# Kernel optimization log

Measured on AMD Instinct MI355X. Metric: run time of the kernel, lower is better.

Reference implementation:

```python
import jax, jax.numpy as jnp
import numpy as np

N, C, K, H = 100000, 128, 16, 4
D = C // H
EPS = 1e-5


def _gelu(x):
    return jax.nn.gelu(x, approximate=False)


def _ln(x, g, b):
    mu = jnp.mean(x, axis=-1, keepdims=True)
    var = jnp.var(x, axis=-1, keepdims=True)
    return (x - mu) * jax.lax.rsqrt(var + EPS) * g + b


def setup_inputs() -> dict:
    key = jax.random.key(0)
    ks = jax.random.split(key, 24)
    s = 0.02
    inp = {
        "feat": jax.random.normal(ks[0], (N, C), jnp.float32),
        "coords": jax.random.normal(ks[1], (N, 3), jnp.float32),
        "knn_idx": jax.random.randint(ks[2], (N, K), 0, N, jnp.int32),
        "Wq": jax.random.normal(ks[3], (C, C), jnp.float32) * s,
        "bq": jnp.zeros((C,), jnp.float32),
        "Wk": jax.random.normal(ks[4], (C, C), jnp.float32) * s,
        "bk": jnp.zeros((C,), jnp.float32),
        "Wv": jax.random.normal(ks[5], (C, C), jnp.float32) * s,
        "bv": jnp.zeros((C,), jnp.float32),
        "Wp1": jax.random.normal(ks[6], (3, C), jnp.float32) * s,
        "bp1": jnp.zeros((C,), jnp.float32),
        "Wp2": jax.random.normal(ks[7], (C, C), jnp.float32) * s,
        "bp2": jnp.zeros((C,), jnp.float32),
        "Wo": jax.random.normal(ks[8], (C, C), jnp.float32) * s,
        "bo": jnp.zeros((C,), jnp.float32),
        "g1": jnp.ones((C,), jnp.float32),
        "b1": jnp.zeros((C,), jnp.float32),
        "Wf1": jax.random.normal(ks[9], (C, 2 * C), jnp.float32) * s,
        "bf1": jnp.zeros((2 * C,), jnp.float32),
        "Wf2": jax.random.normal(ks[10], (2 * C, C), jnp.float32) * s,
        "bf2": jnp.zeros((C,), jnp.float32),
        "g2": jnp.ones((C,), jnp.float32),
        "b2": jnp.zeros((C,), jnp.float32),
    }
    return inp


def reference(feat, coords, knn_idx, Wq, bq, Wk, bk, Wv, bv, Wp1, bp1, Wp2, bp2,
              Wo, bo, g1, b1, Wf1, bf1, Wf2, bf2, g2, b2):
    q = feat @ Wq + bq                      # (N, C)
    k_feat = feat @ Wk + bk
    v_feat = feat @ Wv + bv
    k_nbr = k_feat[knn_idx]                 # (N, K, C) irregular gather
    v_nbr = v_feat[knn_idx]
    rel_pos = coords[knn_idx] - coords[:, None, :]   # (N, K, 3)
    pe = _gelu(rel_pos @ Wp1 + bp1) @ Wp2 + bp2      # (N, K, C)
    k_nbr = (k_nbr + pe).reshape(N, K, H, D)
    v_nbr = (v_nbr + pe).reshape(N, K, H, D)
    qh = q.reshape(N, H, D)
    attn = jnp.einsum('nhd,nkhd->nhk', qh, k_nbr) / jnp.sqrt(jnp.float32(D))
    attn = jax.nn.softmax(attn, axis=-1)    # softmax over the K neighbors
    out = jnp.einsum('nhk,nkhd->nhd', attn, v_nbr).reshape(N, C)
    out = out @ Wo + bo
    x = _ln(feat + out, g1, b1)
    ffn = _gelu(x @ Wf1 + bf1) @ Wf2 + bf2
    return _ln(x + ffn, g2, b2)
```

## Files before the change

### kernel.cpp

```cpp
#include <hip/hip_runtime.h>
#include <math.h>

#define NPTS 100000
#define KNN  16
#define CH   50000
#define NCHUNK 2
#define ATT_BLOCKS 1280

typedef unsigned short bf16;
typedef __attribute__((ext_vector_type(8))) short bf16x8;
typedef __attribute__((ext_vector_type(4))) float f32x4;

__device__ __forceinline__ float bf2f(bf16 v) {
    union { unsigned int u; float f; } x; x.u = ((unsigned int)v) << 16; return x.f;
}
__device__ __forceinline__ bf16 f2bf(float f) {
    union { float f; unsigned int u; } x; x.f = f;
    unsigned int r = (x.u + 0x7FFFu + ((x.u >> 16) & 1u)) >> 16;
    return (bf16)r;
}
__device__ __forceinline__ unsigned int pack_bf16(float lo, float hi) {
    union { float f; unsigned int u; } a, b; a.f = lo; b.f = hi;
    return ((b.u + 0x8000u) & 0xffff0000u) | ((a.u + 0x8000u) >> 16);
}
__device__ __forceinline__ float f_lo(unsigned int u) {
    union { unsigned int x; float f; } c; c.x = u << 16; return c.f;
}
__device__ __forceinline__ float f_hi(unsigned int u) {
    union { unsigned int x; float f; } c; c.x = u & 0xffff0000u; return c.f;
}
__device__ __forceinline__ float ld1(const float* p) { return *p; }
__device__ __forceinline__ float ld1(const bf16* p) { return bf2f(*p); }

__device__ __forceinline__ float gelu_f(float x) {
    return 0.5f * x * (1.0f + erff(x * 0.70710678118654752f));
}
__device__ __forceinline__ float gelu_poly(float t) {
    float w = t * t;
    float poly = fmaf(w, fmaf(w, 0.025f, -0.16666667f), 1.0f);
    return t * fmaf(0.3989423f * t, poly, 0.5f);
}

__global__ void prep1_kernel(const float* __restrict__ Wp2, const float* __restrict__ Wo,
                             const float* __restrict__ bo, const float* __restrict__ bp2,
                             const float* __restrict__ bq, const float* __restrict__ bk,
                             const float* __restrict__ bv,
                             float* __restrict__ Wcat2, float* __restrict__ bo2,
                             float* __restrict__ bcat) {
    int b = blockIdx.x, t = threadIdx.x;
    if (b < 512) {
        int h = b >> 7, j = b & 127;
        float s = 0.f;
        for (int d = 0; d < 32; d++)
            s += Wp2[j * 128 + h * 32 + d] * Wo[(h * 32 + d) * 128 + t];
        Wcat2[b * 128 + t] = s;
    } else if (b == 512) {
        float s = bo[t];
        for (int c = 0; c < 128; c++) s += bp2[c] * Wo[c * 128 + t];
        bo2[t] = s;
    } else {
        bcat[t] = bq[t]; bcat[128 + t] = bk[t]; bcat[256 + t] = bv[t];
    }
}

__global__ void prep2_kernel(const float* __restrict__ Wq, const float* __restrict__ Wk,
                             const float* __restrict__ Wv, const float* __restrict__ Wp2,
                             const float* __restrict__ Wo, const float* __restrict__ Wcat2,
                             const float* __restrict__ Wf1, const float* __restrict__ Wf2,
                             bf16* __restrict__ BcatT, bf16* __restrict__ W2TT,
                             bf16* __restrict__ WcatT, bf16* __restrict__ Wf1T,
                             bf16* __restrict__ Wf2T) {
    int b = blockIdx.x, t = threadIdx.x;
    if (b < 384) {
        const float* W = (b < 128) ? Wq : (b < 256) ? Wk : Wv;
        BcatT[b * 128 + t] = f2bf(W[t * 128 + (b & 127)]);
    } else if (b < 512) {
        int idx = b - 384, h = idx >> 5, d = idx & 31;
        W2TT[h * 4096 + t * 32 + d] = f2bf(Wp2[t * 128 + h * 32 + d]);
    } else if (b < 640) {
        int j = b - 512;
        for (int i = 0; i < 5; i++) {
            int r = t + 128 * i;
            float v = (r < 128) ? Wo[r * 128 + j] : Wcat2[(r - 128) * 128 + j];
            WcatT[j * 640 + r] = f2bf(v);
        }
    } else if (b < 896) {
        int n = b - 640;
        Wf1T[n * 128 + t] = f2bf(Wf1[t * 256 + n]);
    } else {
        int n = b - 896;
        for (int i = 0; i < 2; i++) {
            int k = t + 128 * i;
            Wf2T[n * 256 + k] = f2bf(Wf2[k * 128 + n]);
        }
    }
}

__global__ __launch_bounds__(256) void qkv3_kernel(
    const float* __restrict__ A, const bf16* __restrict__ BT,
    const float* __restrict__ bias, bf16* __restrict__ C, int Nrows)
{
    __shared__ bf16 As[2][128 * 72];
    __shared__ bf16 Bs[2][128 * 72];

    const int tid = threadIdx.x;
    const int row0 = blockIdx.x * 128;
    const int wave = tid >> 6, wr = wave >> 1, wc = wave & 1;
    const int l = tid & 63, l15 = l & 15, g = l >> 4;
    const int sr = tid >> 1;
    const int sh = (tid & 1) * 32;

    {
        int row = row0 + sr;
#pragma unroll
        for (int h = 0; h < 2; h++) {
            uint4 t[4];
            if (row < Nrows) {
                const float* s = A + (size_t)row * 128 + h * 64 + sh;
#pragma unroll
                for (int j2 = 0; j2 < 4; j2++) {
                    float4 a = ((const float4*)s)[2 * j2];
                    float4 b = ((const float4*)s)[2 * j2 + 1];
                    union { uint4 u; ushort4 hh[2]; } c;
                    c.hh[0] = make_ushort4(f2bf(a.x), f2bf(a.y), f2bf(a.z), f2bf(a.w));
                    c.hh[1] = make_ushort4(f2bf(b.x), f2bf(b.y), f2bf(b.z), f2bf(b.w));
                    t[j2] = c.u;
                }
            } else {
#pragma unroll
                for (int j2 = 0; j2 < 4; j2++) t[j2] = make_uint4(0, 0, 0, 0);
            }
            bf16* dst = As[h] + sr * 72 + sh;
#pragma unroll
            for (int j2 = 0; j2 < 4; j2++) *(uint4*)(dst + 8 * j2) = t[j2];
        }
    }
    {
#pragma unroll
        for (int h = 0; h < 2; h++) {
            const bf16* s = BT + (size_t)sr * 128 + h * 64 + sh;
            bf16* dst = Bs[h] + sr * 72 + sh;
#pragma unroll
            for (int j2 = 0; j2 < 4; j2++)
                *(uint4*)(dst + 8 * j2) = ((const uint4*)s)[j2];
        }
    }
    __syncthreads();

    union FragU { uint2 q2[2]; bf16x8 v; };

    for (int z = 0; z < 3; z++) {
        f32x4 acc[4][4];
#pragma unroll
        for (int i = 0; i < 4; i++)
#pragma unroll
            for (int j = 0; j < 4; j++) acc[i][j] = (f32x4){0.f, 0.f, 0.f, 0.f};

#pragma unroll
        for (int h = 0; h < 2; h++) {
#pragma unroll
            for (int s2 = 0; s2 < 2; s2++) {
                bf16x8 af[4], bfr[4];
#pragma unroll
                for (int mt = 0; mt < 4; mt++) {
                    const bf16* p = As[h] + (wr * 64 + mt * 16 + l15) * 72 + s2 * 32 + 4 * g;
                    FragU u; u.q2[0] = *(const uint2*)p; u.q2[1] = *(const uint2*)(p + 16);
                    af[mt] = u.v;
                }
#pragma unroll
                for (int nt = 0; nt < 4; nt++) {
                    const bf16* p = Bs[h] + (wc * 64 + nt * 16 + l15) * 72 + s2 * 32 + 4 * g;
                    FragU u; u.q2[0] = *(const uint2*)p; u.q2[1] = *(const uint2*)(p + 16);
                    bfr[nt] = u.v;
                }
#pragma unroll
                for (int mt = 0; mt < 4; mt++)
#pragma unroll
                    for (int nt = 0; nt < 4; nt++)
                        acc[mt][nt] = __builtin_amdgcn_mfma_f32_16x16x32_bf16(
                            bfr[nt], af[mt], acc[mt][nt], 0, 0, 0);
            }
        }

        const int cg = 4 * g;
        bf16* Cz = C + (size_t)z * NPTS * 128;
        const float* bz = bias + z * 128;
#pragma unroll
        for (int nt = 0; nt < 4; nt++) {
            const int col = wc * 64 + nt * 16 + cg;
            float4 bv4 = *(const float4*)(bz + col);
#pragma unroll
            for (int mt = 0; mt < 4; mt++) {
                int row = row0 + wr * 64 + mt * 16 + l15;
                if (row < Nrows) {
                    float t0 = acc[mt][nt][0] + bv4.x;
                    float t1 = acc[mt][nt][1] + bv4.y;
                    float t2 = acc[mt][nt][2] + bv4.z;
                    float t3 = acc[mt][nt][3] + bv4.w;
                    uint2 u; u.x = pack_bf16(t0, t1); u.y = pack_bf16(t2, t3);
                    *(uint2*)(Cz + (size_t)row * 128 + col) = u;
                }
            }
        }
        __syncthreads();
        if (z < 2) {
#pragma unroll
            for (int h = 0; h < 2; h++) {
                const bf16* s = BT + (size_t)((z + 1) * 128 + sr) * 128 + h * 64 + sh;
                bf16* dst = Bs[h] + sr * 72 + sh;
#pragma unroll
                for (int j2 = 0; j2 < 4; j2++)
                    *(uint4*)(dst + 8 * j2) = ((const uint4*)s)[j2];
            }
            __syncthreads();
        }
    }
}

template<int EPI, bool SPLITA, typename TA, typename TC, typename TR>
__global__ __launch_bounds__(256) void mfma_gemm(
    const TA* __restrict__ A, const bf16* __restrict__ A2,
    const bf16* __restrict__ BT, const float* __restrict__ bias,
    const TR* __restrict__ resid, const float* __restrict__ gamma,
    const float* __restrict__ beta, TC* __restrict__ Cc,
    int Nrows, int Kdim, int lda, int ldc,
    int zA, int zBT, int zbias, int zC)
{
    __shared__ bf16 As[128 * 36];
    __shared__ bf16 Bs[128 * 36];

    const int tid = threadIdx.x;
    const int z = blockIdx.z;
    const TA* Ab = A + (size_t)z * zA;
    const bf16* BTb = BT + (size_t)z * zBT;
    const float* biasb = bias + (size_t)z * zbias;
    TC* Cb = Cc + (size_t)z * zC;

    const int row0 = blockIdx.x * 128;
    const int col0 = blockIdx.y * 128;
    const int wave = tid >> 6, wr = wave >> 1, wc = wave & 1;
    const int l = tid & 63, l15 = l & 15, g = l >> 4;
    const int ar = tid >> 1;
    const int ah = (tid & 1) * 16;

    f32x4 acc[4][4];
#pragma unroll
    for (int i = 0; i < 4; i++)
#pragma unroll
        for (int j = 0; j < 4; j++) acc[i][j] = (f32x4){0.f, 0.f, 0.f, 0.f};

    for (int k0 = 0; k0 < Kdim; k0 += 32) {
        {
            int row = row0 + ar;
            ushort4 tmp[4];
            if (row < Nrows) {
                const bf16* s = (const bf16*)Ab + (size_t)row * lda + k0 + ah;
#pragma unroll
                for (int j = 0; j < 4; j++) tmp[j] = ((const ushort4*)s)[j];
            } else {
#pragma unroll
                for (int j = 0; j < 4; j++) tmp[j] = make_ushort4(0, 0, 0, 0);
            }
#pragma unroll
            for (int j = 0; j < 4; j++)
                *(ushort4*)(As + ar * 36 + ah + 4 * j) = tmp[j];
        }
        {
            int n = col0 + ar;
            const bf16* s = BTb + (size_t)n * Kdim + k0 + ah;
#pragma unroll
            for (int j = 0; j < 4; j++)
                *(ushort4*)(Bs + ar * 36 + ah + 4 * j) = ((const ushort4*)s)[j];
        }
        __syncthreads();

        union FragU { uint2 q2[2]; bf16x8 v; };
        bf16x8 af[4], bfr[4];
#pragma unroll
        for (int mt = 0; mt < 4; mt++) {
            const bf16* p = As + (wr * 64 + mt * 16 + l15) * 36 + 4 * g;
            FragU u; u.q2[0] = *(const uint2*)p; u.q2[1] = *(const uint2*)(p + 16);
            af[mt] = u.v;
        }
#pragma unroll
        for (int nt = 0; nt < 4; nt++) {
            const bf16* p = Bs + (wc * 64 + nt * 16 + l15) * 36 + 4 * g;
            FragU u; u.q2[0] = *(const uint2*)p; u.q2[1] = *(const uint2*)(p + 16);
            bfr[nt] = u.v;
        }
#pragma unroll
        for (int mt = 0; mt < 4; mt++)
#pragma unroll
            for (int nt = 0; nt < 4; nt++)
                acc[mt][nt] = __builtin_amdgcn_mfma_f32_16x16x32_bf16(
                    bfr[nt], af[mt], acc[mt][nt], 0, 0, 0);
        __syncthreads();
    }

    const int cg = 4 * g;
#pragma unroll
    for (int nt = 0; nt < 4; nt++) {
        const int col = col0 + wc * 64 + nt * 16 + cg;
        float4 bv4 = make_float4(0.f, 0.f, 0.f, 0.f);
        if constexpr (EPI >= 1) bv4 = *(const float4*)(biasb + col);
#pragma unroll
        for (int mt = 0; mt < 4; mt++) {
            int row = row0 + wr * 64 + mt * 16 + l15;
            if (row < Nrows) {
                float t0 = acc[mt][nt][0], t1 = acc[mt][nt][1];
                float t2 = acc[mt][nt][2], t3 = acc[mt][nt][3];
                if constexpr (EPI >= 1) { t0 += bv4.x; t1 += bv4.y; t2 += bv4.z; t3 += bv4.w; }
                if constexpr (EPI == 2) { t0 = gelu_f(t0); t1 = gelu_f(t1); t2 = gelu_f(t2); t3 = gelu_f(t3); }
                if constexpr (sizeof(TC) == 2) {
                    uint2 u; u.x = pack_bf16(t0, t1); u.y = pack_bf16(t2, t3);
                    *(uint2*)((bf16*)Cb + (size_t)row * ldc + col) = u;
                } else {
                    *(float4*)((float*)Cb + (size_t)row * ldc + col) = make_float4(t0, t1, t2, t3);
                }
            }
        }
    }
}

template<int EPI, bool SPLITA, typename TA, typename TC, typename TR>
__global__ __launch_bounds__(256) void mfma_gemm64(
    const TA* __restrict__ A, const bf16* __restrict__ A2,
    const bf16* __restrict__ BT, const float* __restrict__ bias,
    const TR* __restrict__ resid, const float* __restrict__ gamma,
    const float* __restrict__ beta, TC* __restrict__ Cc,
    int Nrows, int Kdim, int lda, int ldc,
    int zA, int zBT, int zbias, int zC)
{
    __shared__ bf16 As[128 * 72];
    __shared__ bf16 Bs[128 * 72];
    __shared__ float reds[256], redq[256];
    __shared__ float mu[128], rstd[128];

    const int tid = threadIdx.x;
    const int z = blockIdx.z;
    const TA* Ab = A + (size_t)z * zA;
    const bf16* BTb = BT + (size_t)z * zBT;
    const float* biasb = bias + (size_t)z * zbias;
    TC* Cb = Cc + (size_t)z * zC;

    const int row0 = blockIdx.x * 128;
    const int col0 = blockIdx.y * 128;
    const int wave = tid >> 6, wr = wave >> 1, wc = wave & 1;
    const int l = tid & 63, l15 = l & 15, g = l >> 4;
    const int sr = tid >> 1;
    const int sh = (tid & 1) * 32;

    f32x4 acc[4][4];
#pragma unroll
    for (int i = 0; i < 4; i++)
#pragma unroll
        for (int j = 0; j < 4; j++) acc[i][j] = (f32x4){0.f, 0.f, 0.f, 0.f};

    for (int k0 = 0; k0 < Kdim; k0 += 64) {
        {
            int row = row0 + sr;
            uint4 t[4];
            if (row < Nrows) {
                if constexpr (SPLITA) {
                    const bf16* s = (k0 < 128)
                        ? ((const bf16*)Ab + (size_t)row * 128 + k0 + sh)
                        : (A2 + (size_t)row * 512 + (k0 - 128) + sh);
#pragma unroll
                    for (int j2 = 0; j2 < 4; j2++) t[j2] = ((const uint4*)s)[j2];
                } else if constexpr (sizeof(TA) == 4) {
                    const float* s = (const float*)Ab + (size_t)row * lda + k0 + sh;
#pragma unroll
                    for (int j2 = 0; j2 < 4; j2++) {
                        float4 a = ((const float4*)s)[2 * j2];
                        float4 b = ((const float4*)s)[2 * j2 + 1];
                        union { uint4 u; ushort4 h[2]; } c;
                        c.h[0] = make_ushort4(f2bf(a.x), f2bf(a.y), f2bf(a.z), f2bf(a.w));
                        c.h[1] = make_ushort4(f2bf(b.x), f2bf(b.y), f2bf(b.z), f2bf(b.w));
                        t[j2] = c.u;
                    }
                } else {
                    const bf16* s = (const bf16*)Ab + (size_t)row * lda + k0 + sh;
#pragma unroll
                    for (int j2 = 0; j2 < 4; j2++) t[j2] = ((const uint4*)s)[j2];
                }
            } else {
#pragma unroll
                for (int j2 = 0; j2 < 4; j2++) t[j2] = make_uint4(0, 0, 0, 0);
            }
            bf16* dst = As + sr * 72 + sh;
#pragma unroll
            for (int j2 = 0; j2 < 4; j2++) *(uint4*)(dst + 8 * j2) = t[j2];
        }
        {
            int nn = col0 + sr;
            const bf16* s = BTb + (size_t)nn * Kdim + k0 + sh;
            uint4 t[4];
#pragma unroll
            for (int j2 = 0; j2 < 4; j2++) t[j2] = ((const uint4*)s)[j2];
            bf16* dst = Bs + sr * 72 + sh;
#pragma unroll
            for (int j2 = 0; j2 < 4; j2++) *(uint4*)(dst + 8 * j2) = t[j2];
        }
        __syncthreads();

        union FragU { uint2 q2[2]; bf16x8 v; };
#pragma unroll
        for (int s = 0; s < 2; s++) {
            bf16x8 af[4], bfr[4];
#pragma unroll
            for (int mt = 0; mt < 4; mt++) {
                const bf16* p = As + (wr * 64 + mt * 16 + l15) * 72 + s * 32 + 4 * g;
                FragU u; u.q2[0] = *(const uint2*)p; u.q2[1] = *(const uint2*)(p + 16);
                af[mt] = u.v;
            }
#pragma unroll
            for (int nt = 0; nt < 4; nt++) {
                const bf16* p = Bs + (wc * 64 + nt * 16 + l15) * 72 + s * 32 + 4 * g;
                FragU u; u.q2[0] = *(const uint2*)p; u.q2[1] = *(const uint2*)(p + 16);
                bfr[nt] = u.v;
            }
#pragma unroll
            for (int mt = 0; mt < 4; mt++)
#pragma unroll
                for (int nt = 0; nt < 4; nt++)
                    acc[mt][nt] = __builtin_amdgcn_mfma_f32_16x16x32_bf16(
                        bfr[nt], af[mt], acc[mt][nt], 0, 0, 0);
        }
        __syncthreads();
    }

    const int cg = 4 * g;

    if constexpr (EPI != 3) {
#pragma unroll
        for (int nt = 0; nt < 4; nt++) {
            const int col = col0 + wc * 64 + nt * 16 + cg;
            float4 bv4 = make_float4(0.f, 0.f, 0.f, 0.f);
            if constexpr (EPI >= 1) bv4 = *(const float4*)(biasb + col);
#pragma unroll
            for (int mt = 0; mt < 4; mt++) {
                int row = row0 + wr * 64 + mt * 16 + l15;
                if (row < Nrows) {
                    float t0 = acc[mt][nt][0], t1 = acc[mt][nt][1];
                    float t2 = acc[mt][nt][2], t3 = acc[mt][nt][3];
                    if constexpr (EPI >= 1) { t0 += bv4.x; t1 += bv4.y; t2 += bv4.z; t3 += bv4.w; }
                    if constexpr (EPI == 2) { t0 = gelu_f(t0); t1 = gelu_f(t1); t2 = gelu_f(t2); t3 = gelu_f(t3); }
                    if constexpr (sizeof(TC) == 2) {
                        uint2 u; u.x = pack_bf16(t0, t1); u.y = pack_bf16(t2, t3);
                        *(uint2*)((bf16*)Cb + (size_t)row * ldc + col) = u;
                    } else {
                        *(float4*)((float*)Cb + (size_t)row * ldc + col) = make_float4(t0, t1, t2, t3);
                    }
                }
            }
        }
    } else {
        float4 bias4[4];
#pragma unroll
        for (int nt = 0; nt < 4; nt++)
            bias4[nt] = *(const float4*)(biasb + wc * 64 + nt * 16 + cg);
#pragma unroll
        for (int mt = 0; mt < 4; mt++) {
            int rl = wr * 64 + mt * 16 + l15;
            int row = row0 + rl;
            float s = 0.f, q = 0.f;
#pragma unroll
            for (int nt = 0; nt < 4; nt++) {
                const int col = wc * 64 + nt * 16 + cg;
                float rv0 = 0.f, rv1 = 0.f, rv2 = 0.f, rv3 = 0.f;
                if (row < Nrows) {
                    if constexpr (sizeof(TR) == 2) {
                        ushort4 rr = *(const ushort4*)((const bf16*)resid + (size_t)row * 128 + col);
                        rv0 = bf2f(rr.x); rv1 = bf2f(rr.y); rv2 = bf2f(rr.z); rv3 = bf2f(rr.w);
                    } else {
                        float4 rr = *(const float4*)((const float*)resid + (size_t)row * 128 + col);
                        rv0 = rr.x; rv1 = rr.y; rv2 = rr.z; rv3 = rr.w;
                    }
                }
                float t0 = acc[mt][nt][0] + bias4[nt].x + rv0;
                float t1 = acc[mt][nt][1] + bias4[nt].y + rv1;
                float t2 = acc[mt][nt][2] + bias4[nt].z + rv2;
                float t3 = acc[mt][nt][3] + bias4[nt].w + rv3;
                acc[mt][nt][0] = t0; acc[mt][nt][1] = t1;
                acc[mt][nt][2] = t2; acc[mt][nt][3] = t3;
                s += t0 + t1 + t2 + t3;
                q = fmaf(t0, t0, q); q = fmaf(t1, t1, q);
                q = fmaf(t2, t2, q); q = fmaf(t3, t3, q);
            }
            s += __shfl_xor(s, 16); s += __shfl_xor(s, 32);
            q += __shfl_xor(q, 16); q += __shfl_xor(q, 32);
            if ((l & 48) == 0) { reds[rl * 2 + wc] = s; redq[rl * 2 + wc] = q; }
        }
        __syncthreads();
        if (tid < 128) {
            float s = reds[tid * 2] + reds[tid * 2 + 1];
            float q = redq[tid * 2] + redq[tid * 2 + 1];
            float m = s * (1.f / 128.f);
            float v = q * (1.f / 128.f) - m * m;
            mu[tid] = m; rstd[tid] = rsqrtf(v + 1e-5f);
        }
        __syncthreads();
        float4 g4[4], b4[4];
#pragma unroll
        for (int nt = 0; nt < 4; nt++) {
            g4[nt] = *(const float4*)(gamma + wc * 64 + nt * 16 + cg);
            b4[nt] = *(const float4*)(beta + wc * 64 + nt * 16 + cg);
        }
#pragma unroll
        for (int mt = 0; mt < 4; mt++) {
            int rl = wr * 64 + mt * 16 + l15;
            int row = row0 + rl;
            if (row < Nrows) {
                float m = mu[rl], rd = rstd[rl];
#pragma unroll
                for (int nt = 0; nt < 4; nt++) {
                    const int col = wc * 64 + nt * 16 + cg;
                    float t0 = (acc[mt][nt][0] - m) * rd * g4[nt].x + b4[nt].x;
                    float t1 = (acc[mt][nt][1] - m) * rd * g4[nt].y + b4[nt].y;
                    float t2 = (acc[mt][nt][2] - m) * rd * g4[nt].z + b4[nt].z;
                    float t3 = (acc[mt][nt][3] - m) * rd * g4[nt].w + b4[nt].w;
                    if constexpr (sizeof(TC) == 2) {
                        uint2 u; u.x = pack_bf16(t0, t1); u.y = pack_bf16(t2, t3);
                        *(uint2*)((bf16*)Cb + (size_t)row * 128 + col) = u;
                    } else {
                        *(float4*)((float*)Cb + (size_t)row * 128 + col) = make_float4(t0, t1, t2, t3);
                    }
                }
            }
        }
    }
}

__global__ __launch_bounds__(256, 5) void attn_kernel(
    const bf16* __restrict__ qx, const bf16* __restrict__ kf,
    const bf16* __restrict__ vf, const bf16* __restrict__ qp,
    const float* __restrict__ coords, const int* __restrict__ knn,
    const float* __restrict__ Wp1, const float* __restrict__ bp1,
    bf16* __restrict__ attn_v, bf16* __restrict__ s_out, int nbase)
{
    __shared__ __align__(16) float W1s[524];
    __shared__ __align__(16) unsigned int hv_s[4][16 * 68];
    __shared__ __align__(16) float qp_s[4][4 * 144];
    __shared__ __align__(16) float a_s[4][64];
    __shared__ int idx_s[4][16];

    const int tid = threadIdx.x;
    if (tid < 128) {
        int c = tid;
        int s4 = 4 * c + 4 * (c >> 5);
        W1s[s4 + 0] = Wp1[c];
        W1s[s4 + 1] = Wp1[128 + c];
        W1s[s4 + 2] = Wp1[256 + c];
        W1s[s4 + 3] = bp1[c];
    }
    __syncthreads();

    const int wv = tid >> 6, l = tid & 63;
    const int k = l >> 2, j = l & 3;
    unsigned int* hv32 = hv_s[wv];
    float* qpsf = qp_s[wv];
    float* as4 = a_s[wv];
    int* ixs = idx_s[wv];
    const float SCALE = 0.17677669529663688f;
    const int wave = blockIdx.x * 4 + wv;
    const int qoff = (l >> 4) * 144 + ((l & 15) >> 2) * 36 + ((l & 15) & 3) * 8;

    for (int n = nbase + wave; n < nbase + CH; n += ATT_BLOCKS * 4) {
        const int idx = knn[n * KNN + k];
        if (j == 0) ixs[k] = idx;
        const float cx = coords[n * 3 + 0], cy = coords[n * 3 + 1], cz = coords[n * 3 + 2];
        const float rx = coords[idx * 3 + 0] - cx;
        const float ry = coords[idx * 3 + 1] - cy;
        const float rz = coords[idx * 3 + 2] - cz;
        {
            uint4 qpr = *(const uint4*)(qp + (size_t)(n - nbase) * 512 + l * 8);
            float4 qa, qb;
            qa.x = f_lo(qpr.x); qa.y = f_hi(qpr.x);
            qa.z = f_lo(qpr.y); qa.w = f_hi(qpr.y);
            qb.x = f_lo(qpr.z); qb.y = f_hi(qpr.z);
            qb.z = f_lo(qpr.w); qb.w = f_hi(qpr.w);
            *(float4*)(qpsf + qoff) = qa;
            *(float4*)(qpsf + qoff + 4) = qb;
        }
        const bf16* krow = kf + (size_t)idx * 128 + j * 32;
        const bf16* qrow = qx + (size_t)n * 128 + j * 32;
        uint4 kw[4], qw[4];
#pragma unroll
        for (int m = 0; m < 4; m++) {
            kw[m] = *(const uint4*)(krow + 8 * m);
            qw[m] = *(const uint4*)(qrow + 8 * m);
        }
        asm volatile("s_waitcnt lgkmcnt(0)" ::: "memory");

        float p0 = 0.f, p1 = 0.f, p2 = 0.f, p3 = 0.f;
        const float* wbase = W1s + 132 * j;
        const int jb = j * 36;
#pragma unroll
        for (int blk = 0; blk < 4; blk++) {
            const int cb = blk * 8;
            float4 q0a = *(const float4*)(qpsf + jb + cb);
            float4 q0b = *(const float4*)(qpsf + jb + cb + 4);
            float4 q1a = *(const float4*)(qpsf + 144 + jb + cb);
            float4 q1b = *(const float4*)(qpsf + 144 + jb + cb + 4);
            float4 q2a = *(const float4*)(qpsf + 288 + jb + cb);
            float4 q2b = *(const float4*)(qpsf + 288 + jb + cb + 4);
            float4 q3a = *(const float4*)(qpsf + 432 + jb + cb);
            float4 q3b = *(const float4*)(qpsf + 432 + jb + cb + 4);
            float gg[8];
#pragma unroll
            for (int i = 0; i < 8; i++) {
                float4 w = *(const float4*)(wbase + 4 * (cb + i));
                float t = fmaf(rx, w.x, fmaf(ry, w.y, fmaf(rz, w.z, w.w)));
                float gv = gelu_poly(t);
                gg[i] = gv;
                float v0 = (i < 4) ? ((const float*)&q0a)[i] : ((const float*)&q0b)[i - 4];
                float v1 = (i < 4) ? ((const float*)&q1a)[i] : ((const float*)&q1b)[i - 4];
                float v2 = (i < 4) ? ((const float*)&q2a)[i] : ((const float*)&q2b)[i - 4];
                float v3 = (i < 4) ? ((const float*)&q3a)[i] : ((const float*)&q3b)[i - 4];
                p0 = fmaf(gv, v0, p0);
                p1 = fmaf(gv, v1, p1);
                p2 = fmaf(gv, v2, p2);
                p3 = fmaf(gv, v3, p3);
            }
            uint4 pk4;
            pk4.x = pack_bf16(gg[0], gg[1]);
            pk4.y = pack_bf16(gg[2], gg[3]);
            pk4.z = pack_bf16(gg[4], gg[5]);
            pk4.w = pack_bf16(gg[6], gg[7]);
            *(uint4*)(hv32 + k * 68 + j * 16 + blk * 4) = pk4;
        }

        float qk = 0.f;
#pragma unroll
        for (int m = 0; m < 4; m++) {
#pragma unroll
            for (int w = 0; w < 4; w++) {
                unsigned int ua = ((const unsigned int*)&kw[m])[w];
                unsigned int ub = ((const unsigned int*)&qw[m])[w];
                qk = fmaf(f_lo(ua), f_lo(ub), qk);
                qk = fmaf(f_hi(ua), f_hi(ub), qk);
            }
        }

        p0 += __shfl_xor(p0, 1); p0 += __shfl_xor(p0, 2);
        p1 += __shfl_xor(p1, 1); p1 += __shfl_xor(p1, 2);
        p2 += __shfl_xor(p2, 1); p2 += __shfl_xor(p2, 2);
        p3 += __shfl_xor(p3, 1); p3 += __shfl_xor(p3, 2);
        float pe = (j == 0) ? p0 : (j == 1) ? p1 : (j == 2) ? p2 : p3;
        float logit = (qk + pe) * SCALE;

        float mx = logit;
#pragma unroll
        for (int off = 4; off <= 32; off <<= 1) mx = fmaxf(mx, __shfl_xor(mx, off));
        float e = __expf(logit - mx);
        float ss = e;
#pragma unroll
        for (int off = 4; off <= 32; off <<= 1) ss += __shfl_xor(ss, off);
        float a = e * __builtin_amdgcn_rcpf(ss);
        as4[k * 4 + j] = a;
        asm volatile("s_waitcnt lgkmcnt(0)" ::: "memory");
        __builtin_amdgcn_sched_barrier(0);

        float ov0 = 0.f, ov1 = 0.f;
        float sv0a = 0.f, sv0b = 0.f, sv1a = 0.f, sv1b = 0.f;
        float sv2a = 0.f, sv2b = 0.f, sv3a = 0.f, sv3b = 0.f;
        const int l4 = l & 16, l5 = l & 32;
#pragma unroll
        for (int kk = 0; kk < 16; kk++) {
            float4 av = *(const float4*)(as4 + kk * 4);
            unsigned int hp = hv32[kk * 68 + l];
            float h_lo = f_lo(hp), h_hi = f_hi(hp);
            sv0a = fmaf(av.x, h_lo, sv0a); sv0b = fmaf(av.x, h_hi, sv0b);
            sv1a = fmaf(av.y, h_lo, sv1a); sv1b = fmaf(av.y, h_hi, sv1b);
            sv2a = fmaf(av.z, h_lo, sv2a); sv2b = fmaf(av.z, h_hi, sv2b);
            sv3a = fmaf(av.w, h_lo, sv3a); sv3b = fmaf(av.w, h_hi, sv3b);
            int ixk = ixs[kk];
            unsigned int vp = *(const unsigned int*)(vf + (size_t)ixk * 128 + 2 * l);
            float v_lo = f_lo(vp), v_hi = f_hi(vp);
            float t01 = l4 ? av.y : av.x;
            float t23 = l4 ? av.w : av.z;
            float ah = l5 ? t23 : t01;
            ov0 = fmaf(ah, v_lo, ov0);
            ov1 = fmaf(ah, v_hi, ov1);
        }
        unsigned int* s32 = (unsigned int*)(s_out + (size_t)(n - nbase) * 512);
        s32[l]        = pack_bf16(sv0a, sv0b);
        s32[64 + l]   = pack_bf16(sv1a, sv1b);
        s32[128 + l]  = pack_bf16(sv2a, sv2b);
        s32[192 + l]  = pack_bf16(sv3a, sv3b);
        *(unsigned int*)(attn_v + (size_t)n * 128 + 2 * l) = pack_bf16(ov0, ov1);
    }
}

__global__ void ws_report_kernel(float* out, int n, float val) {
    int i = blockIdx.x * 256 + threadIdx.x;
    if (i < n) out[i] = val;
}

extern "C" void kernel_launch(void* const* d_in, const int* in_sizes, int n_in,
                              void* d_out, int out_size, void* d_ws, size_t ws_size,
                              hipStream_t stream) {
    const float* feat   = (const float*)d_in[0];
    const float* coords = (const float*)d_in[1];
    const int*   knn    = (const int*)d_in[2];
    const float* Wq  = (const float*)d_in[3];  const float* bq  = (const float*)d_in[4];
    const float* Wk  = (const float*)d_in[5];  const float* bk  = (const float*)d_in[6];
    const float* Wv  = (const float*)d_in[7];  const float* bv  = (const float*)d_in[8];
    const float* Wp1 = (const float*)d_in[9];  const float* bp1 = (const float*)d_in[10];
    const float* Wp2 = (const float*)d_in[11]; const float* bp2 = (const float*)d_in[12];
    const float* Wo  = (const float*)d_in[13]; const float* bo  = (const float*)d_in[14];
    const float* g1  = (const float*)d_in[15]; const float* b1  = (const float*)d_in[16];
    const float* Wf1 = (const float*)d_in[17]; const float* bf1 = (const float*)d_in[18];
    const float* Wf2 = (const float*)d_in[19]; const float* bf2 = (const float*)d_in[20];
    const float* g2  = (const float*)d_in[21]; const float* b2  = (const float*)d_in[22];

    bf16* qx = (bf16*)d_ws;
    bf16* kb = qx + (size_t)NPTS * 128;
    bf16* vb = kb + (size_t)NPTS * 128;
    bf16* BcatT = vb + (size_t)NPTS * 128;
    bf16* W2TT  = BcatT + 384 * 128;
    bf16* WcatT = W2TT + 4 * 128 * 32;
    bf16* Wf1T  = WcatT + 128 * 640;
    bf16* Wf2T  = Wf1T + 256 * 128;
    float* Wcat2 = (float*)(Wf2T + 128 * 256);
    float* bo2   = Wcat2 + 512 * 128;
    float* bcat  = bo2 + 128;

    const size_t needed = ((size_t)NPTS * 128 * 3 + 384 * 128 + 4 * 128 * 32 + 128 * 640
                           + 256 * 128 + 128 * 256) * 2
                        + (512 * 128 + 128 + 384) * 4;
    if (ws_size < needed) {
        float val = 1000.0f + (float)((double)ws_size / 1073741824.0);
        hipLaunchKernelGGL(ws_report_kernel, dim3((out_size + 255) / 256), dim3(256), 0, stream,
                           (float*)d_out, out_size, val);
        return;
    }

    dim3 blk(256);
    const int GN = (NPTS + 127) / 128;
    const int GC = (CH + 127) / 128;

    hipLaunchKernelGGL(prep1_kernel, dim3(514), dim3(128), 0, stream,
                       Wp2, Wo, bo, bp2, bq, bk, bv, Wcat2, bo2, bcat);
    hipLaunchKernelGGL(prep2_kernel, dim3(1024), dim3(128), 0, stream,
                       Wq, Wk, Wv, Wp2, Wo, Wcat2, Wf1, Wf2,
                       BcatT, W2TT, WcatT, Wf1T, Wf2T);

    hipLaunchKernelGGL(qkv3_kernel, dim3(GN), blk, 0, stream,
                       feat, BcatT, bcat, qx, NPTS);

    bf16* qpb = (bf16*)d_out;

    for (int c = 0; c < NCHUNK; c++) {
        const int base = c * CH;
        hipLaunchKernelGGL((mfma_gemm<0, false, bf16, bf16, float>),
                           dim3(GC, 1, 4), blk, 0, stream,
                           qx + (size_t)base * 128, nullptr, W2TT, nullptr,
                           nullptr, nullptr, nullptr, qpb,
                           CH, 32, 128, 512, 32, 128 * 32, 0, 128);
        hipLaunchKernelGGL(attn_kernel, dim3(ATT_BLOCKS), blk, 0, stream,
                           qx, kb, vb, qpb, coords, knn, Wp1, bp1,
                           qx, qpb, base);
        hipLaunchKernelGGL((mfma_gemm64<3, true, bf16, bf16, float>),
                           dim3(GC, 1, 1), blk, 0, stream,
                           qx + (size_t)base * 128, qpb, WcatT, bo2,
                           feat + (size_t)base * 128, g1, b1, qx + (size_t)base * 128,
                           CH, 640, 128, 128, 0, 0, 0, 0);
    }

    hipLaunchKernelGGL((mfma_gemm64<2, false, bf16, bf16, float>),
                       dim3(GN, 2, 1), blk, 0, stream,
                       qx, nullptr, Wf1T, bf1, nullptr, nullptr, nullptr, kb,
                       NPTS, 128, 128, 256, 0, 0, 0, 0);

    hipLaunchKernelGGL((mfma_gemm64<3, false, bf16, float, bf16>),
                       dim3(GN, 1, 1), blk, 0, stream,
                       kb, nullptr, Wf2T, bf2, qx, g2, b2, (float*)d_out,
                       NPTS, 256, 256, 128, 0, 0, 0, 0);
}
```

Before: 432.1 us.

## Fuse FFN GEMMs, GELU and final LayerNorm into one kernel

Replaces the two separate FFN GEMM launches with a single kernel that keeps a 128-row tile of x in shared memory. It computes the hidden layer in 64-column slices with GELU into LDS and accumulates the second GEMM directly, then applies bias, residual and LayerNorm in the epilogue. This removes the round trip of the 100000x256 bf16 hidden activation through global memory and one launch. In exchange it uses large LDS per block, which lowers occupancy, and the weight slices are reloaded serially with extra barriers per slice.

Measured after the change: 410.2 us. 5.1% less time.

```diff
diff --git a/kernel.cpp b/kernel.cpp
--- a/kernel.cpp
+++ b/kernel.cpp
@@ -29,8 +29,6 @@
 __device__ __forceinline__ float f_hi(unsigned int u) {
     union { unsigned int x; float f; } c; c.x = u & 0xffff0000u; return c.f;
 }
-__device__ __forceinline__ float ld1(const float* p) { return *p; }
-__device__ __forceinline__ float ld1(const bf16* p) { return bf2f(*p); }
 
 __device__ __forceinline__ float gelu_f(float x) {
     return 0.5f * x * (1.0f + erff(x * 0.70710678118654752f));
@@ -217,6 +215,204 @@
     }
 }
 
+__global__ __launch_bounds__(256) void ffn_fused_kernel(
+    const bf16* __restrict__ X, const bf16* __restrict__ Wf1T,
+    const bf16* __restrict__ Wf2T, const float* __restrict__ bf1,
+    const float* __restrict__ bf2, const float* __restrict__ gamma,
+    const float* __restrict__ beta, float* __restrict__ Out, int Nrows)
+{
+    __shared__ bf16 Xs[2][128 * 72];
+    __shared__ bf16 Bs[9216];
+    __shared__ bf16 Us[128 * 72];
+    __shared__ float reds[256], redq[256], mu[128], rstd[128];
+
+    const int tid = threadIdx.x;
+    const int row0 = blockIdx.x * 128;
+    const int wave = tid >> 6, wr = wave >> 1, wc = wave & 1;
+    const int l = tid & 63, l15 = l & 15, g = l >> 4;
+
+    {
+        const int sr = tid >> 1, sh = (tid & 1) * 32;
+        int row = row0 + sr;
+#pragma unroll
+        for (int h = 0; h < 2; h++) {
+            uint4 t[4];
+            if (row < Nrows) {
+                const bf16* s = X + (size_t)row * 128 + h * 64 + sh;
+#pragma unroll
+                for (int j2 = 0; j2 < 4; j2++) t[j2] = ((const uint4*)s)[j2];
+            } else {
+#pragma unroll
+                for (int j2 = 0; j2 < 4; j2++) t[j2] = make_uint4(0, 0, 0, 0);
+            }
+            bf16* dst = Xs[h] + sr * 72 + sh;
+#pragma unroll
+            for (int j2 = 0; j2 < 4; j2++) *(uint4*)(dst + 8 * j2) = t[j2];
+        }
+    }
+
+    union FragU { uint2 q2[2]; bf16x8 v; };
+
+    f32x4 acc2[4][4];
+#pragma unroll
+    for (int i = 0; i < 4; i++)
+#pragma unroll
+        for (int j = 0; j < 4; j++) acc2[i][j] = (f32x4){0.f, 0.f, 0.f, 0.f};
+
+    for (int p = 0; p < 4; p++) {
+        __syncthreads();
+        {
+            const int r = tid >> 2, q = tid & 3;
+            const int h = q >> 1, sub = (q & 1) * 32;
+            const bf16* s = Wf1T + (size_t)(p * 64 + r) * 128 + h * 64 + sub;
+            bf16* dst = Bs + h * 4608 + r * 72 + sub;
+#pragma unroll
+            for (int j2 = 0; j2 < 4; j2++)
+                *(uint4*)(dst + 8 * j2) = ((const uint4*)s)[j2];
+        }
+        __syncthreads();
+        f32x4 acc1[2][4];
+#pragma unroll
+        for (int i = 0; i < 2; i++)
+#pragma unroll
+            for (int j = 0; j < 4; j++) acc1[i][j] = (f32x4){0.f, 0.f, 0.f, 0.f};
+#pragma unroll
+        for (int h = 0; h < 2; h++) {
+#pragma unroll
+            for (int s2 = 0; s2 < 2; s2++) {
+                bf16x8 af[2], bfr[4];
+#pragma unroll
+                for (int mt = 0; mt < 2; mt++) {
+                    const bf16* pp = Xs[h] + (wave * 32 + mt * 16 + l15) * 72 + s2 * 32 + 4 * g;
+                    FragU u; u.q2[0] = *(const uint2*)pp; u.q2[1] = *(const uint2*)(pp + 16);
+                    af[mt] = u.v;
+                }
+#pragma unroll
+                for (int nt = 0; nt < 4; nt++) {
+                    const bf16* pp = Bs + h * 4608 + (nt * 16 + l15) * 72 + s2 * 32 + 4 * g;
+                    FragU u; u.q2[0] = *(const uint2*)pp; u.q2[1] = *(const uint2*)(pp + 16);
+                    bfr[nt] = u.v;
+                }
+#pragma unroll
+                for (int mt = 0; mt < 2; mt++)
+#pragma unroll
+                    for (int nt = 0; nt < 4; nt++)
+                        acc1[mt][nt] = __builtin_amdgcn_mfma_f32_16x16x32_bf16(
+                            bfr[nt], af[mt], acc1[mt][nt], 0, 0, 0);
+            }
+        }
+        {
+            const int cg = 4 * g;
+#pragma unroll
+            for (int nt = 0; nt < 4; nt++) {
+                const int col = nt * 16 + cg;
+                float4 bv4 = *(const float4*)(bf1 + p * 64 + col);
+#pragma unroll
+                for (int mt = 0; mt < 2; mt++) {
+                    float t0 = gelu_f(acc1[mt][nt][0] + bv4.x);
+                    float t1 = gelu_f(acc1[mt][nt][1] + bv4.y);
+                    float t2 = gelu_f(acc1[mt][nt][2] + bv4.z);
+                    float t3 = gelu_f(acc1[mt][nt][3] + bv4.w);
+                    uint2 u; u.x = pack_bf16(t0, t1); u.y = pack_bf16(t2, t3);
+                    *(uint2*)(Us + (wave * 32 + mt * 16 + l15) * 72 + col) = u;
+                }
+            }
+        }
+        __syncthreads();
+        {
+            const int r = tid >> 1, kh = tid & 1;
+            const bf16* s = Wf2T + (size_t)r * 256 + p * 64 + kh * 32;
+            bf16* dst = Bs + kh * 4608 + r * 36;
+            *(uint4*)(dst) = ((const uint4*)s)[0];
+            *(uint4*)(dst + 8) = ((const uint4*)s)[1];
+            *(uint4*)(dst + 16) = ((const uint4*)s)[2];
+            *(uint4*)(dst + 24) = ((const uint4*)s)[3];
+        }
+        __syncthreads();
+#pragma unroll
+        for (int s2 = 0; s2 < 2; s2++) {
+            bf16x8 af2[4], bfr2[4];
+#pragma unroll
+            for (int mt = 0; mt < 4; mt++) {
+                const bf16* pp = Us + (wr * 64 + mt * 16 + l15) * 72 + s2 * 32 + 4 * g;
+                FragU u; u.q2[0] = *(const uint2*)pp; u.q2[1] = *(const uint2*)(pp + 16);
+                af2[mt] = u.v;
+            }
+#pragma unroll
+            for (int nt = 0; nt < 4; nt++) {
+                const bf16* pp = Bs + s2 * 4608 + (wc * 64 + nt * 16 + l15) * 36 + 4 * g;
+                FragU u; u.q2[0] = *(const uint2*)pp; u.q2[1] = *(const uint2*)(pp + 16);
+                bfr2[nt] = u.v;
+            }
+#pragma unroll
+            for (int mt = 0; mt < 4; mt++)
+#pragma unroll
+                for (int nt = 0; nt < 4; nt++)
+                    acc2[mt][nt] = __builtin_amdgcn_mfma_f32_16x16x32_bf16(
+                        bfr2[nt], af2[mt], acc2[mt][nt], 0, 0, 0);
+        }
+    }
+
+    const int cg = 4 * g;
+    float4 bias4[4];
+#pragma unroll
+    for (int nt = 0; nt < 4; nt++)
+        bias4[nt] = *(const float4*)(bf2 + wc * 64 + nt * 16 + cg);
+#pragma unroll
+    for (int mt = 0; mt < 4; mt++) {
+        int rl = wr * 64 + mt * 16 + l15;
+        float s = 0.f, q = 0.f;
+#pragma unroll
+        for (int nt = 0; nt < 4; nt++) {
+            uint2 rp = *(const uint2*)(Xs[wc] + rl * 72 + nt * 16 + cg);
+            float t0 = acc2[mt][nt][0] + bias4[nt].x + f_lo(rp.x);
+            float t1 = acc2[mt][nt][1] + bias4[nt].y + f_hi(rp.x);
+            float t2 = acc2[mt][nt][2] + bias4[nt].z + f_lo(rp.y);
+            float t3 = acc2[mt][nt][3] + bias4[nt].w + f_hi(rp.y);
+            acc2[mt][nt][0] = t0; acc2[mt][nt][1] = t1;
+            acc2[mt][nt][2] = t2; acc2[mt][nt][3] = t3;
+            s += t0 + t1 + t2 + t3;
+            q = fmaf(t0, t0, q); q = fmaf(t1, t1, q);
+            q = fmaf(t2, t2, q); q = fmaf(t3, t3, q);
+        }
+        s += __shfl_xor(s, 16); s += __shfl_xor(s, 32);
+        q += __shfl_xor(q, 16); q += __shfl_xor(q, 32);
+        if ((l & 48) == 0) { reds[rl * 2 + wc] = s; redq[rl * 2 + wc] = q; }
+    }
+    __syncthreads();
+    if (tid < 128) {
+        float s = reds[tid * 2] + reds[tid * 2 + 1];
+        float q = redq[tid * 2] + redq[tid * 2 + 1];
+        float m = s * (1.f / 128.f);
+        float v = q * (1.f / 128.f) - m * m;
+        mu[tid] = m; rstd[tid] = rsqrtf(v + 1e-5f);
+    }
+    __syncthreads();
+    float4 g4[4], b4[4];
+#pragma unroll
+    for (int nt = 0; nt < 4; nt++) {
+        g4[nt] = *(const float4*)(gamma + wc * 64 + nt * 16 + cg);
+        b4[nt] = *(const float4*)(beta + wc * 64 + nt * 16 + cg);
+    }
+#pragma unroll
+    for (int mt = 0; mt < 4; mt++) {
+        int rl = wr * 64 + mt * 16 + l15;
+        int row = row0 + rl;
+        if (row < Nrows) {
+            float m = mu[rl], rd = rstd[rl];
+#pragma unroll
+            for (int nt = 0; nt < 4; nt++) {
+                const int col = wc * 64 + nt * 16 + cg;
+                float t0 = (acc2[mt][nt][0] - m) * rd * g4[nt].x + b4[nt].x;
+                float t1 = (acc2[mt][nt][1] - m) * rd * g4[nt].y + b4[nt].y;
+                float t2 = (acc2[mt][nt][2] - m) * rd * g4[nt].z + b4[nt].z;
+                float t3 = (acc2[mt][nt][3] - m) * rd * g4[nt].w + b4[nt].w;
+                *(float4*)(Out + (size_t)row * 128 + col) = make_float4(t0, t1, t2, t3);
+            }
+        }
+    }
+}
+
 template<int EPI, bool SPLITA, typename TA, typename TC, typename TR>
 __global__ __launch_bounds__(256) void mfma_gemm(
     const TA* __restrict__ A, const bf16* __restrict__ A2,
@@ -768,13 +964,6 @@
                            CH, 640, 128, 128, 0, 0, 0, 0);
     }
 
-    hipLaunchKernelGGL((mfma_gemm64<2, false, bf16, bf16, float>),
-                       dim3(GN, 2, 1), blk, 0, stream,
-                       qx, nullptr, Wf1T, bf1, nullptr, nullptr, nullptr, kb,
-                       NPTS, 128, 128, 256, 0, 0, 0, 0);
-
-    hipLaunchKernelGGL((mfma_gemm64<3, false, bf16, float, bf16>),
-                       dim3(GN, 1, 1), blk, 0, stream,
-                       kb, nullptr, Wf2T, bf2, qx, g2, b2, (float*)d_out,
-                       NPTS, 256, 256, 128, 0, 0, 0, 0);
-}
+    hipLaunchKernelGGL(ffn_fused_kernel, dim3(GN), blk, 0, stream,
+                       qx, Wf1T, Wf2T, bf1, bf2, g2, b2, (float*)d_out, NPTS);
+}
```
